# Performance work log

Hardware: AMD Instinct MI355X
Metric: run time of the kernel (lower is better)

The kernel has to match this reference:

```python
import jax, jax.numpy as jnp
import numpy as np

B, T, C, H = 128, 512, 128, 64  # batch, seq, n_embd, head_size


def setup_inputs() -> dict:
    key = jax.random.key(0)
    ks = jax.random.split(key, 6)
    s = 1.0 / np.sqrt(C)
    return {
        "x": jax.random.normal(ks[0], (B, T, C), dtype=jnp.float32),
        "Wg": jax.random.normal(ks[1], (C, C), dtype=jnp.float32) * s,
        "bg": jnp.zeros((C,), dtype=jnp.float32),
        "Wk": jax.random.normal(ks[2], (C, H), dtype=jnp.float32) * s,
        "Wq": jax.random.normal(ks[3], (C, H), dtype=jnp.float32) * s,
        "Wv": jax.random.normal(ks[4], (C, H), dtype=jnp.float32) * s,
    }


def reference(x, Wg, bg, Wk, Wq, Wv):
    # GateLayer: x * sigmoid(Linear(x))
    g = jax.nn.sigmoid(jnp.einsum('btc,cd->btd', x, Wg) + bg)
    xg = x * g
    k = jnp.einsum('btc,ch->bth', xg, Wk)
    q = jnp.einsum('btc,ch->bth', xg, Wq)
    v = jnp.einsum('btc,ch->bth', xg, Wv)
    # NOTE: original scales by C**-0.5 (n_embd), not head_size**-0.5
    scale = C ** -0.5
    wei = jnp.einsum('bqh,bkh->bqk', q, k) * scale  # [B,T,T]
    causal = jnp.tril(jnp.ones((T, T), dtype=bool))
    wei = jnp.where(causal, wei, -jnp.inf)
    wei = jax.nn.softmax(wei, axis=-1)
    # dropout is identity in eval mode
    out = jnp.einsum('bqk,bkh->bqh', wei, v)  # [B,T,H]
    return out
```

## Files before the change

### kernel.cpp

```cpp
#include <hip/hip_runtime.h>


#define BB 128
#define TB 512
#define CC 128
#define HH 64

static constexpr float SCALE = 0.088388347648318447f;

typedef __attribute__((ext_vector_type(8))) short bf16x8;
typedef __attribute__((ext_vector_type(8))) unsigned short u16x8;
typedef __attribute__((ext_vector_type(4))) float f32x4;

__device__ inline unsigned short f2bf(float f) {
    union { float f; unsigned u; } x; x.f = f;
    unsigned r = x.u + 0x7fff + ((x.u >> 16) & 1);
    return (unsigned short)(r >> 16);
}
__device__ inline float bf2f(unsigned short h) {
    union { unsigned u; float f; } x; x.u = ((unsigned)h) << 16;
    return x.f;
}

__global__ void prep_weights(const float* __restrict__ Wg, const float* __restrict__ Wk,
                             const float* __restrict__ Wq, const float* __restrict__ Wv,
                             unsigned short* __restrict__ WgT, unsigned short* __restrict__ WkT,
                             unsigned short* __restrict__ WqT, unsigned short* __restrict__ WvT)
{
    int idx = blockIdx.x * 256 + threadIdx.x;
    if (idx < 16384) {
        int n = idx >> 7, k = idx & 127;
        WgT[idx] = f2bf(Wg[k * CC + n]);
    } else {
        int j = idx - 16384;
        int mtx = j >> 13;
        int r = j & 8191;
        int n = r >> 7, k = r & 127;
        const float* W = (mtx == 0) ? Wk : (mtx == 1) ? Wq : Wv;
        unsigned short* WT = (mtx == 0) ? WkT : (mtx == 1) ? WqT : WvT;
        WT[r] = f2bf(W[k * HH + n]);
    }
}

__global__ __launch_bounds__(256, 2) void gate_qkv_kernel(
    const float* __restrict__ x, const float* __restrict__ bg,
    const unsigned short* __restrict__ WgT, const unsigned short* __restrict__ WkT,
    const unsigned short* __restrict__ WqT, const unsigned short* __restrict__ WvT,
    unsigned short* __restrict__ qo, unsigned short* __restrict__ ko,
    unsigned short* __restrict__ vto)
{
    __shared__ unsigned short xsb[128 * 136];

    const int tid  = threadIdx.x;
    const int wv   = tid >> 6;
    const int lane = tid & 63;
    const int l15  = lane & 15;
    const int quad = lane >> 4;
    const int R0   = blockIdx.x * 128;

#pragma unroll
    for (int it = 0; it < 16; ++it) {
        int fid = tid + 256 * it;
        int r = fid >> 5, c4 = fid & 31;
        float4 xv = *(const float4*)(x + (size_t)(R0 + r) * CC + c4 * 4);
        ushort4 h;
        h.x = f2bf(xv.x); h.y = f2bf(xv.y); h.z = f2bf(xv.z); h.w = f2bf(xv.w);
        *(ushort4*)(xsb + r * 136 + c4 * 4) = h;
    }
    __syncthreads();

    bf16x8 bx[2][4];
#pragma unroll
    for (int mt = 0; mt < 2; ++mt)
#pragma unroll
        for (int kc = 0; kc < 4; ++kc)
            bx[mt][kc] = *(const bf16x8*)(xsb + (32 * wv + 16 * mt + l15) * 136 +
                                          kc * 32 + quad * 8);

    f32x4 acc[8][2];
#pragma unroll
    for (int nt = 0; nt < 8; ++nt)
#pragma unroll
        for (int mt = 0; mt < 2; ++mt) acc[nt][mt] = (f32x4){0.f, 0.f, 0.f, 0.f};

    bf16x8 awA[4], awB[4];
#pragma unroll
    for (int kc = 0; kc < 4; ++kc)
        awA[kc] = *(const bf16x8*)(WgT + l15 * CC + kc * 32 + quad * 8);

#pragma unroll
    for (int nt = 0; nt < 8; ++nt) {
        if (nt < 7) {
#pragma unroll
            for (int kc = 0; kc < 4; ++kc)
                awB[kc] = *(const bf16x8*)(WgT + (16 * (nt + 1) + l15) * CC + kc * 32 + quad * 8);
        } else {
#pragma unroll
            for (int kc = 0; kc < 4; ++kc)
                awB[kc] = *(const bf16x8*)(WkT + l15 * CC + kc * 32 + quad * 8);
        }
#pragma unroll
        for (int mt = 0; mt < 2; ++mt)
#pragma unroll
            for (int kc = 0; kc < 4; ++kc)
                acc[nt][mt] = __builtin_amdgcn_mfma_f32_16x16x32_bf16(
                    awA[kc], bx[mt][kc], acc[nt][mt], 0, 0, 0);
#pragma unroll
        for (int kc = 0; kc < 4; ++kc) awA[kc] = awB[kc];
    }

#pragma unroll
    for (int nt = 0; nt < 8; ++nt) {
        float4 bgv = *(const float4*)(bg + 16 * nt + quad * 4);
#pragma unroll
        for (int mt = 0; mt < 2; ++mt) {
            int m = 32 * wv + 16 * mt + l15;
            unsigned short* p = xsb + m * 136 + 16 * nt + quad * 4;
            ushort4 xb = *(const ushort4*)p;
            float e0 = __expf(-(acc[nt][mt][0] + bgv.x));
            float e1 = __expf(-(acc[nt][mt][1] + bgv.y));
            float e2 = __expf(-(acc[nt][mt][2] + bgv.z));
            float e3 = __expf(-(acc[nt][mt][3] + bgv.w));
            ushort4 o;
            o.x = f2bf(bf2f(xb.x) * __builtin_amdgcn_rcpf(1.f + e0));
            o.y = f2bf(bf2f(xb.y) * __builtin_amdgcn_rcpf(1.f + e1));
            o.z = f2bf(bf2f(xb.z) * __builtin_amdgcn_rcpf(1.f + e2));
            o.w = f2bf(bf2f(xb.w) * __builtin_amdgcn_rcpf(1.f + e3));
            *(ushort4*)p = o;
        }
    }
    __syncthreads();

#pragma unroll
    for (int mt = 0; mt < 2; ++mt)
#pragma unroll
        for (int kc = 0; kc < 4; ++kc)
            bx[mt][kc] = *(const bf16x8*)(xsb + (32 * wv + 16 * mt + l15) * 136 +
                                          kc * 32 + quad * 8);

    const int b = R0 >> 9, t0 = R0 & 511;
#pragma unroll
    for (int pj = 0; pj < 3; ++pj) {
        f32x4 pacc[4][2];
#pragma unroll
        for (int nt = 0; nt < 4; ++nt)
#pragma unroll
            for (int mt = 0; mt < 2; ++mt) pacc[nt][mt] = (f32x4){0.f, 0.f, 0.f, 0.f};

#pragma unroll
        for (int nt = 0; nt < 4; ++nt) {
            if (!(pj == 2 && nt == 3)) {
                const unsigned short* Wcur = (pj == 0) ? WkT : (pj == 1) ? WqT : WvT;
                const unsigned short* Wnxt = (pj == 0) ? WqT : WvT;
                const unsigned short* Wp   = (nt < 3) ? Wcur : Wnxt;
                const int ntn = (nt < 3) ? nt + 1 : 0;
#pragma unroll
                for (int kc = 0; kc < 4; ++kc)
                    awB[kc] = *(const bf16x8*)(Wp + (16 * ntn + l15) * CC + kc * 32 + quad * 8);
            }
#pragma unroll
            for (int mt = 0; mt < 2; ++mt)
#pragma unroll
                for (int kc = 0; kc < 4; ++kc)
                    pacc[nt][mt] = __builtin_amdgcn_mfma_f32_16x16x32_bf16(
                        awA[kc], bx[mt][kc], pacc[nt][mt], 0, 0, 0);
#pragma unroll
            for (int kc = 0; kc < 4; ++kc) awA[kc] = awB[kc];
        }

        if (pj < 2) {
            unsigned short* O = (pj == 0) ? ko : qo;
#pragma unroll
            for (int nt = 0; nt < 4; ++nt)
#pragma unroll
                for (int mt = 0; mt < 2; ++mt) {
                    int m = 32 * wv + 16 * mt + l15;
                    ushort4 h;
                    h.x = f2bf(pacc[nt][mt][0]); h.y = f2bf(pacc[nt][mt][1]);
                    h.z = f2bf(pacc[nt][mt][2]); h.w = f2bf(pacc[nt][mt][3]);
                    *(ushort4*)(O + (size_t)(R0 + m) * HH + 16 * nt + quad * 4) = h;
                }
        } else {
#pragma unroll
            for (int nt = 0; nt < 4; ++nt)
#pragma unroll
                for (int mt = 0; mt < 2; ++mt) {
                    int m = 32 * wv + 16 * mt + l15;
                    unsigned short* dst =
                        vto + (size_t)b * (HH * TB) + (16 * nt + quad * 4) * TB + t0 + m;
#pragma unroll
                    for (int r = 0; r < 4; ++r)
                        dst[r * TB] = f2bf(pacc[nt][mt][r]);
                }
        }
    }
}

__device__ __forceinline__ void pv_nomax(const f32x4* s, f32x4& lacc, f32x4* o4,
                                         unsigned short* ps, const bf16x8* bv0,
                                         const bf16x8* bv1, const bf16x8 ones,
                                         int wave, int l15, int quad)
{
#pragma unroll
    for (int nt = 0; nt < 4; ++nt)
#pragma unroll
        for (int r = 0; r < 4; ++r)
            ps[(16 * wave + quad * 4 + r) * 76 + 16 * nt + l15] = f2bf(__expf(s[nt][r]));

    bf16x8 ap0 = *(const bf16x8*)(ps + (16 * wave + l15) * 76 + quad * 8);
    bf16x8 ap1 = *(const bf16x8*)(ps + (16 * wave + l15) * 76 + 32 + quad * 8);
    lacc = __builtin_amdgcn_mfma_f32_16x16x32_bf16(ap0, ones, lacc, 0, 0, 0);
    lacc = __builtin_amdgcn_mfma_f32_16x16x32_bf16(ap1, ones, lacc, 0, 0, 0);
#pragma unroll
    for (int nt = 0; nt < 4; ++nt) {
        o4[nt] = __builtin_amdgcn_mfma_f32_16x16x32_bf16(ap0, bv0[nt], o4[nt], 0, 0, 0);
        o4[nt] = __builtin_amdgcn_mfma_f32_16x16x32_bf16(ap1, bv1[nt], o4[nt], 0, 0, 0);
    }
}

__device__ __forceinline__ void attn_epilogue(const f32x4* o4, const f32x4 lacc,
                                              float* out, size_t base, int q0,
                                              int wave, int l15, int quad)
{
    float inv[4];
#pragma unroll
    for (int r = 0; r < 4; ++r) inv[r] = __builtin_amdgcn_rcpf(lacc[r]);
#pragma unroll
    for (int nt = 0; nt < 4; ++nt)
#pragma unroll
        for (int r = 0; r < 4; ++r)
            out[base + (size_t)(q0 + 16 * wave + quad * 4 + r) * HH + 16 * nt + l15] =
                o4[nt][r] * inv[r];
}

__global__ __launch_bounds__(256, 2) void attn_kernel(
    const unsigned short* __restrict__ q, const unsigned short* __restrict__ k,
    const unsigned short* __restrict__ vt, float* __restrict__ out)
{
    __shared__ unsigned short ks[64 * 72];
    __shared__ unsigned short vs[64 * 72];
    __shared__ unsigned short ps[64 * 76];

    const int tid  = threadIdx.x;
    const int wave = tid >> 6;
    const int lane = tid & 63;
    const int l15  = lane & 15;
    const int quad = lane >> 4;
    const int pr   = blockIdx.x;
    const int b    = blockIdx.y;
    const size_t base = (size_t)b * TB * HH;

    const int qtA = pr, qtB = 7 - pr;
    const int q0A = qtA * 64, q0B = qtB * 64;

    bf16x8 ones;
#pragma unroll
    for (int i = 0; i < 8; ++i) ones[i] = (short)0x3F80;

    const int r0 = tid >> 3, c8 = (tid & 7) * 8;
    const int r1 = r0 + 32;

    bf16x8 kr0 = *(const bf16x8*)(k + base + (size_t)r0 * HH + c8);
    bf16x8 kr1 = *(const bf16x8*)(k + base + (size_t)r1 * HH + c8);
    bf16x8 vr0 = *(const bf16x8*)(vt + base + (size_t)r0 * TB + c8);
    bf16x8 vr1 = *(const bf16x8*)(vt + base + (size_t)r1 * TB + c8);

    const unsigned short* qrA = q + base + (size_t)(q0A + 16 * wave + l15) * HH;
    const unsigned short* qrB = q + base + (size_t)(q0B + 16 * wave + l15) * HH;
    bf16x8 aqA0 = *(const bf16x8*)(qrA + quad * 8);
    bf16x8 aqA1 = *(const bf16x8*)(qrA + 32 + quad * 8);
    bf16x8 aqB0 = *(const bf16x8*)(qrB + quad * 8);
    bf16x8 aqB1 = *(const bf16x8*)(qrB + 32 + quad * 8);

    f32x4 oA[4], oB[4], lAacc, lBacc;
#pragma unroll
    for (int nt = 0; nt < 4; ++nt) {
        oA[nt] = (f32x4){0.f, 0.f, 0.f, 0.f};
        oB[nt] = (f32x4){0.f, 0.f, 0.f, 0.f};
    }
    lAacc = (f32x4){0.f, 0.f, 0.f, 0.f};
    lBacc = (f32x4){0.f, 0.f, 0.f, 0.f};

    const int nIt = qtB + 1;
    for (int kt = 0; kt < nIt; ++kt) {
        __syncthreads();
        *(bf16x8*)(ks + r0 * 72 + c8) = kr0;
        *(bf16x8*)(ks + r1 * 72 + c8) = kr1;
        *(bf16x8*)(vs + r0 * 72 + c8) = vr0;
        *(bf16x8*)(vs + r1 * 72 + c8) = vr1;
        __syncthreads();

        if (kt + 1 < nIt) {
            const int k0n = (kt + 1) * 64;
            kr0 = *(const bf16x8*)(k + base + (size_t)(k0n + r0) * HH + c8);
            kr1 = *(const bf16x8*)(k + base + (size_t)(k0n + r1) * HH + c8);
            vr0 = *(const bf16x8*)(vt + base + (size_t)r0 * TB + k0n + c8);
            vr1 = *(const bf16x8*)(vt + base + (size_t)r1 * TB + k0n + c8);
        }

        bf16x8 bk0[4], bk1[4], bv0[4], bv1[4];
#pragma unroll
        for (int nt = 0; nt < 4; ++nt) {
            bk0[nt] = *(const bf16x8*)(ks + (16 * nt + l15) * 72 + quad * 8);
            bk1[nt] = *(const bf16x8*)(ks + (16 * nt + l15) * 72 + 32 + quad * 8);
            bv0[nt] = *(const bf16x8*)(vs + (16 * nt + l15) * 72 + quad * 8);
            bv1[nt] = *(const bf16x8*)(vs + (16 * nt + l15) * 72 + 32 + quad * 8);
        }

        const bool actA = (kt <= qtA);

        f32x4 sA[4], sB[4];
#pragma unroll
        for (int nt = 0; nt < 4; ++nt) {
            f32x4 zb = (f32x4){0.f, 0.f, 0.f, 0.f};
            zb = __builtin_amdgcn_mfma_f32_16x16x32_bf16(aqB0, bk0[nt], zb, 0, 0, 0);
            zb = __builtin_amdgcn_mfma_f32_16x16x32_bf16(aqB1, bk1[nt], zb, 0, 0, 0);
            sB[nt] = zb;
            if (actA) {
                f32x4 za = (f32x4){0.f, 0.f, 0.f, 0.f};
                za = __builtin_amdgcn_mfma_f32_16x16x32_bf16(aqA0, bk0[nt], za, 0, 0, 0);
                za = __builtin_amdgcn_mfma_f32_16x16x32_bf16(aqA1, bk1[nt], za, 0, 0, 0);
                sA[nt] = za;
            }
        }

        if (actA) {
            const bool diagA = (kt == qtA);
#pragma unroll
            for (int nt = 0; nt < 4; ++nt)
#pragma unroll
                for (int r = 0; r < 4; ++r) {
                    float sv = sA[nt][r] * SCALE;
                    if (diagA && (16 * nt + l15) > (16 * wave + quad * 4 + r)) sv = -1e30f;
                    sA[nt][r] = sv;
                }
            pv_nomax(sA, lAacc, oA, ps, bv0, bv1, ones, wave, l15, quad);
            if (diagA) attn_epilogue(oA, lAacc, out, base, q0A, wave, l15, quad);
        }

        {
            const bool diagB = (kt == qtB);
#pragma unroll
            for (int nt = 0; nt < 4; ++nt)
#pragma unroll
                for (int r = 0; r < 4; ++r) {
                    float sv = sB[nt][r] * SCALE;
                    if (diagB && (16 * nt + l15) > (16 * wave + quad * 4 + r)) sv = -1e30f;
                    sB[nt][r] = sv;
                }
            pv_nomax(sB, lBacc, oB, ps, bv0, bv1, ones, wave, l15, quad);
        }
    }

    attn_epilogue(oB, lBacc, out, base, q0B, wave, l15, quad);
}

extern "C" void kernel_launch(void* const* d_in, const int* in_sizes, int n_in,
                              void* d_out, int out_size, void* d_ws, size_t ws_size,
                              hipStream_t stream) {
    const float* x  = (const float*)d_in[0];
    const float* Wg = (const float*)d_in[1];
    const float* bg = (const float*)d_in[2];
    const float* Wk = (const float*)d_in[3];
    const float* Wq = (const float*)d_in[4];
    const float* Wv = (const float*)d_in[5];
    float* out = (float*)d_out;

    unsigned short* ws = (unsigned short*)d_ws;
    const size_t BTH = (size_t)BB * TB * HH;
    unsigned short* qo  = ws;
    unsigned short* ko  = ws + BTH;
    unsigned short* vto = ws + 2 * BTH;
    unsigned short* WgT = ws + 3 * BTH;
    unsigned short* WkT = WgT + 16384;
    unsigned short* WqT = WkT + 8192;
    unsigned short* WvT = WqT + 8192;

    hipLaunchKernelGGL(prep_weights, dim3(160), dim3(256), 0, stream,
                       Wg, Wk, Wq, Wv, WgT, WkT, WqT, WvT);
    hipLaunchKernelGGL(gate_qkv_kernel, dim3(BB * TB / 128), dim3(256), 0, stream,
                       x, bg, WgT, WkT, WqT, WvT, qo, ko, vto);
    hipLaunchKernelGGL(attn_kernel, dim3(4, BB), dim3(256), 0, stream,
                       qo, ko, vto, out);
}
```

Before: 129.4 us.

## Load x directly into registers per wave and stage V transpose through LDS

Each wave now loads its own rows of x from global memory straight into MFMA fragments, plus fp32 copies for the gate multiply. This removes the block-wide LDS staging of x and both __syncthreads barriers. The gated activations are written to per-wave LDS rows and read back only by the same wave. The transposed V output is first parked in a per-wave LDS tile and then written out as contiguous 16-byte stores, replacing strided 2-byte scattered global writes. The cost is more registers for the held x values, extra LDS, and possibly misaligned 16-byte LDS reads, since the 34-element row pitch is not 16-byte aligned.

Result: slower. 132.1 us (+2.1%).

```diff
diff --git a/kernel.cpp b/kernel.cpp
--- a/kernel.cpp
+++ b/kernel.cpp
@@ -20,6 +20,14 @@
 __device__ inline float bf2f(unsigned short h) {
     union { unsigned u; float f; } x; x.u = ((unsigned)h) << 16;
     return x.f;
+}
+__device__ inline bf16x8 pack8(float4 a, float4 b) {
+    bf16x8 o;
+    o[0] = (short)f2bf(a.x); o[1] = (short)f2bf(a.y);
+    o[2] = (short)f2bf(a.z); o[3] = (short)f2bf(a.w);
+    o[4] = (short)f2bf(b.x); o[5] = (short)f2bf(b.y);
+    o[6] = (short)f2bf(b.z); o[7] = (short)f2bf(b.w);
+    return o;
 }
 
 __global__ void prep_weights(const float* __restrict__ Wg, const float* __restrict__ Wk,
@@ -49,7 +57,8 @@
     unsigned short* __restrict__ qo, unsigned short* __restrict__ ko,
     unsigned short* __restrict__ vto)
 {
-    __shared__ unsigned short xsb[128 * 136];
+    __shared__ unsigned short xgs[128 * 136];
+    __shared__ unsigned short vpark[4 * 64 * 34];
 
     const int tid  = threadIdx.x;
     const int wv   = tid >> 6;
@@ -57,25 +66,26 @@
     const int l15  = lane & 15;
     const int quad = lane >> 4;
     const int R0   = blockIdx.x * 128;
-
-#pragma unroll
-    for (int it = 0; it < 16; ++it) {
-        int fid = tid + 256 * it;
-        int r = fid >> 5, c4 = fid & 31;
-        float4 xv = *(const float4*)(x + (size_t)(R0 + r) * CC + c4 * 4);
-        ushort4 h;
-        h.x = f2bf(xv.x); h.y = f2bf(xv.y); h.z = f2bf(xv.z); h.w = f2bf(xv.w);
-        *(ushort4*)(xsb + r * 136 + c4 * 4) = h;
-    }
-    __syncthreads();
+    const int row0 = R0 + 32 * wv;
 
     bf16x8 bx[2][4];
 #pragma unroll
     for (int mt = 0; mt < 2; ++mt)
 #pragma unroll
-        for (int kc = 0; kc < 4; ++kc)
-            bx[mt][kc] = *(const bf16x8*)(xsb + (32 * wv + 16 * mt + l15) * 136 +
-                                          kc * 32 + quad * 8);
+        for (int kc = 0; kc < 4; ++kc) {
+            const float* p = x + (size_t)(row0 + 16 * mt + l15) * CC + kc * 32 + quad * 8;
+            float4 a = *(const float4*)p;
+            float4 c = *(const float4*)(p + 4);
+            bx[mt][kc] = pack8(a, c);
+        }
+
+    float4 xe[8][2];
+#pragma unroll
+    for (int nt = 0; nt < 8; ++nt)
+#pragma unroll
+        for (int mt = 0; mt < 2; ++mt)
+            xe[nt][mt] = *(const float4*)(x + (size_t)(row0 + 16 * mt + l15) * CC +
+                                          16 * nt + 4 * quad);
 
     f32x4 acc[8][2];
 #pragma unroll
@@ -111,34 +121,33 @@
 
 #pragma unroll
     for (int nt = 0; nt < 8; ++nt) {
-        float4 bgv = *(const float4*)(bg + 16 * nt + quad * 4);
+        float4 bgv = *(const float4*)(bg + 16 * nt + 4 * quad);
 #pragma unroll
         for (int mt = 0; mt < 2; ++mt) {
             int m = 32 * wv + 16 * mt + l15;
-            unsigned short* p = xsb + m * 136 + 16 * nt + quad * 4;
-            ushort4 xb = *(const ushort4*)p;
             float e0 = __expf(-(acc[nt][mt][0] + bgv.x));
             float e1 = __expf(-(acc[nt][mt][1] + bgv.y));
             float e2 = __expf(-(acc[nt][mt][2] + bgv.z));
             float e3 = __expf(-(acc[nt][mt][3] + bgv.w));
             ushort4 o;
-            o.x = f2bf(bf2f(xb.x) * __builtin_amdgcn_rcpf(1.f + e0));
-            o.y = f2bf(bf2f(xb.y) * __builtin_amdgcn_rcpf(1.f + e1));
-            o.z = f2bf(bf2f(xb.z) * __builtin_amdgcn_rcpf(1.f + e2));
-            o.w = f2bf(bf2f(xb.w) * __builtin_amdgcn_rcpf(1.f + e3));
-            *(ushort4*)p = o;
-        }
-    }
-    __syncthreads();
-
+            o.x = f2bf(xe[nt][mt].x * __builtin_amdgcn_rcpf(1.f + e0));
+            o.y = f2bf(xe[nt][mt].y * __builtin_amdgcn_rcpf(1.f + e1));
+            o.z = f2bf(xe[nt][mt].z * __builtin_amdgcn_rcpf(1.f + e2));
+            o.w = f2bf(xe[nt][mt].w * __builtin_amdgcn_rcpf(1.f + e3));
+            *(ushort4*)(xgs + m * 136 + 16 * nt + 4 * quad) = o;
+        }
+    }
+
+    bf16x8 bxg[2][4];
 #pragma unroll
     for (int mt = 0; mt < 2; ++mt)
 #pragma unroll
         for (int kc = 0; kc < 4; ++kc)
-            bx[mt][kc] = *(const bf16x8*)(xsb + (32 * wv + 16 * mt + l15) * 136 +
-                                          kc * 32 + quad * 8);
+            bxg[mt][kc] = *(const bf16x8*)(xgs + (32 * wv + 16 * mt + l15) * 136 +
+                                           kc * 32 + quad * 8);
 
     const int b = R0 >> 9, t0 = R0 & 511;
+    unsigned short* vp = vpark + wv * (64 * 34);
 #pragma unroll
     for (int pj = 0; pj < 3; ++pj) {
         f32x4 pacc[4][2];
@@ -163,7 +172,7 @@
 #pragma unroll
                 for (int kc = 0; kc < 4; ++kc)
                     pacc[nt][mt] = __builtin_amdgcn_mfma_f32_16x16x32_bf16(
-                        awA[kc], bx[mt][kc], pacc[nt][mt], 0, 0, 0);
+                        awA[kc], bxg[mt][kc], pacc[nt][mt], 0, 0, 0);
 #pragma unroll
             for (int kc = 0; kc < 4; ++kc) awA[kc] = awB[kc];
         }
@@ -185,13 +194,18 @@
             for (int nt = 0; nt < 4; ++nt)
 #pragma unroll
                 for (int mt = 0; mt < 2; ++mt) {
-                    int m = 32 * wv + 16 * mt + l15;
-                    unsigned short* dst =
-                        vto + (size_t)b * (HH * TB) + (16 * nt + quad * 4) * TB + t0 + m;
+                    int tloc = 16 * mt + l15;
 #pragma unroll
                     for (int r = 0; r < 4; ++r)
-                        dst[r * TB] = f2bf(pacc[nt][mt][r]);
+                        vp[(16 * nt + 4 * quad + r) * 34 + tloc] = f2bf(pacc[nt][mt][r]);
                 }
+            unsigned short* dst = vto + (size_t)b * (HH * TB) + (size_t)lane * TB +
+                                  t0 + 32 * wv;
+#pragma unroll
+            for (int c = 0; c < 4; ++c) {
+                u16x8 vv = *(const u16x8*)(vp + lane * 34 + 8 * c);
+                *(u16x8*)(dst + 8 * c) = vv;
+            }
         }
     }
 }
```
